# Kernel optimization log

Hardware: AMD Instinct MI355X
Metric: run time of the kernel (lower is better)

Reference implementation:

```python
import jax, jax.numpy as jnp
import numpy as np

N_NODES = 50000
N_EDGES = 1000000


def _edge_conv(x, src, dst, W, b, n_nodes):
    """PyG EdgeConv: msg = nn(cat([x_i, x_j - x_i])), aggr=max over incoming edges."""
    xi = x[dst]                      # [E, C] target features
    xj = x[src]                      # [E, C] source features
    m = jnp.concatenate([xi, xj - xi], axis=-1)          # [E, 2C]
    m = jax.nn.relu(m @ W + b)                           # [E, C_out]
    out = jax.ops.segment_max(m, dst, num_segments=n_nodes)  # [N, C_out]
    # empty segments produce -inf; PyG fills with 0
    return jnp.where(jnp.isfinite(out), out, 0.0)


def setup_inputs() -> dict:
    key = jax.random.key(0)
    ks = jax.random.split(key, 12)
    x = jax.random.normal(ks[0], (N_NODES, 3), dtype=jnp.float32)
    edge_index = jax.random.randint(ks[1], (2, N_EDGES), 0, N_NODES, dtype=jnp.int64)

    def lin(k, fan_in, fan_out):
        s = 1.0 / np.sqrt(fan_in)
        kw, kb = jax.random.split(k)
        W = jax.random.uniform(kw, (fan_in, fan_out), jnp.float32, -s, s)
        b = jax.random.uniform(kb, (fan_out,), jnp.float32, -s, s)
        return W, b

    W1, b1 = lin(ks[2], 6, 64)       # conv1 MLP([3*2, 64])
    W2, b2 = lin(ks[3], 128, 128)    # conv2 MLP([64*2, 128])
    W3, b3 = lin(ks[4], 256, 512)    # conv3 MLP([128*2, 512])
    W4, b4 = lin(ks[5], 512, 256)    # lin1 MLP([512, 256])
    W5, b5 = lin(ks[6], 256, 3)      # lin1 final Linear(256, 3)
    return {"x": x, "edge_index": edge_index,
            "W1": W1, "b1": b1, "W2": W2, "b2": b2, "W3": W3, "b3": b3,
            "W4": W4, "b4": b4, "W5": W5, "b5": b5}


def reference(x, edge_index, W1, b1, W2, b2, W3, b3, W4, b4, W5, b5):
    src = edge_index[0]  # x_j
    dst = edge_index[1]  # x_i (aggregation target)
    n = x.shape[0]
    x1 = _edge_conv(x, src, dst, W1, b1, n)    # [N, 64]
    x2 = _edge_conv(x1, src, dst, W2, b2, n)   # [N, 128]
    x3 = _edge_conv(x2, src, dst, W3, b3, n)   # [N, 512]
    x4 = jax.nn.relu(x3 @ W4 + b4) @ W5 + b5   # [N, 3]
    return x + x4
```

## Files before the change

kernel.cpp:

```cpp
#include <hip/hip_runtime.h>

static constexpr int NN = 50000;
static constexpr int NE = 1000000;

typedef short bf16x8 __attribute__((ext_vector_type(8)));
typedef float f32x4 __attribute__((ext_vector_type(4)));

__device__ inline float bf2f_raw(unsigned short u) {
    return __uint_as_float(((unsigned int)u) << 16);
}
__device__ inline unsigned short f2bf(float f) {
    unsigned int u = __float_as_uint(f);
    u += 0x7fffu + ((u >> 16) & 1u);
    return (unsigned short)(u >> 16);
}
__device__ inline void fmax2(float& a0, float& a1, unsigned int v) {
    a0 = fmaxf(a0, bf2f_raw((unsigned short)(v & 0xffffu)));
    a1 = fmaxf(a1, bf2f_raw((unsigned short)(v >> 16)));
}
__device__ inline unsigned int pack2(float f0, float f1) {
    return (unsigned int)f2bf(f0) | ((unsigned int)f2bf(f1) << 16);
}
__device__ inline unsigned int addrelu2(unsigned int a, float t0, float t1) {
    float f0 = fmaxf(bf2f_raw((unsigned short)(a & 0xffffu)) + t0, 0.f);
    float f1 = fmaxf(bf2f_raw((unsigned short)(a >> 16)) + t1, 0.f);
    return pack2(f0, f1);
}


__global__ void setup_kernel(const float* __restrict__ x, const float* __restrict__ W1,
                             const float* __restrict__ b1, const float* __restrict__ b5,
                             const float* __restrict__ W2, const float* __restrict__ W3,
                             const float* __restrict__ W4,
                             unsigned short* __restrict__ as1, float* __restrict__ out,
                             int* __restrict__ deg, int* __restrict__ cursor,
                             unsigned short* __restrict__ Bt2,
                             unsigned short* __restrict__ Bt3,
                             unsigned short* __restrict__ W4t) {
    int t = blockIdx.x * blockDim.x + threadIdx.x;
    if (t < NN * 128) {
        int i = t >> 7, c = t & 127;
        float x0 = x[i * 3 + 0], x1 = x[i * 3 + 1], x2 = x[i * 3 + 2];
        float v;
        if (c < 64) {
            v = x0 * (W1[c] - W1[192 + c]) + x1 * (W1[64 + c] - W1[256 + c]) +
                x2 * (W1[128 + c] - W1[320 + c]) + b1[c];
        } else {
            int cs = c - 64;
            v = x0 * W1[192 + cs] + x1 * W1[256 + cs] + x2 * W1[320 + cs];
        }
        as1[t] = f2bf(v);
        return;
    }
    t -= NN * 128;
    if (t < NN * 3) { out[t] = x[t] + b5[t % 3]; return; }
    t -= NN * 3;
    if (t < NN) { deg[t] = 0; return; }
    t -= NN;
    if (t < NN) { cursor[t] = 0; return; }
    t -= NN;
    if (t < 8192) {
        int k = t / 128, c = t % 128;
        float wt = W2[k * 128 + c];
        float wb = W2[(64 + k) * 128 + c];
        Bt2[c * 64 + k] = f2bf(wt - wb);
        Bt2[(128 + c) * 64 + k] = f2bf(wb);
        return;
    }
    t -= 8192;
    if (t < 65536) {
        int k = t / 512, c = t % 512;
        float wt = W3[k * 512 + c];
        float wb = W3[(128 + k) * 512 + c];
        Bt3[c * 128 + k] = f2bf(wt - wb);
        Bt3[(512 + c) * 128 + k] = f2bf(wb);
        return;
    }
    t -= 65536;
    if (t < 131072) {
        int k = t / 256, n = t % 256;
        W4t[n * 512 + k] = f2bf(W4[k * 256 + n]);
    }
}


__global__ void hist_kernel(const int* __restrict__ dst, int* __restrict__ deg) {
    int e = blockIdx.x * blockDim.x + threadIdx.x;
    if (e < NE) atomicAdd(&deg[dst[e]], 1);
}

__global__ __launch_bounds__(1024) void scan_kernel(const int* __restrict__ deg,
                                                    int* __restrict__ rowstart) {
    __shared__ int wave_sums[16];
    constexpr int CH = (NN + 1023) / 1024;
    int tid = threadIdx.x;
    int lane = tid & 63;
    int wave = tid >> 6;
    int base = tid * CH;
    int vals[CH];
    int sum = 0;
    #pragma unroll
    for (int i = 0; i < CH; ++i) {
        int idx = base + i;
        vals[i] = (idx < NN) ? deg[idx] : 0;
        sum += vals[i];
    }
    int x = sum;
    #pragma unroll
    for (int off = 1; off < 64; off <<= 1) {
        int y = __shfl_up(x, off);
        if (lane >= off) x += y;
    }
    if (lane == 63) wave_sums[wave] = x;
    __syncthreads();
    if (wave == 0 && lane < 16) {
        int s = wave_sums[lane];
        #pragma unroll
        for (int off = 1; off < 16; off <<= 1) {
            int y = __shfl_up(s, off);
            if (lane >= off) s += y;
        }
        wave_sums[lane] = s;
    }
    __syncthreads();
    int run = (wave ? wave_sums[wave - 1] : 0) + x - sum;
    #pragma unroll
    for (int i = 0; i < CH; ++i) {
        int idx = base + i;
        if (idx < NN) rowstart[idx] = run;
        run += vals[i];
    }
    if (tid == 1023) rowstart[NN] = run;
}

__global__ void scatter_kernel(const int* __restrict__ src, const int* __restrict__ dst,
                               const int* __restrict__ rowstart, int* __restrict__ cursor,
                               int* __restrict__ csr) {
    int e = blockIdx.x * blockDim.x + threadIdx.x;
    if (e < NE) {
        int d = dst[e];
        int pos = atomicAdd(&cursor[d], 1);
        csr[rowstart[d] + pos] = src[e];
    }
}


__global__ __launch_bounds__(256) void edge_fused_conv1_kernel(
    const unsigned short* __restrict__ as, const int* __restrict__ rowstart,
    const int* __restrict__ csr, unsigned short* __restrict__ x1) {
    int wid = (blockIdx.x * 256 + threadIdx.x) >> 6;
    int lane = threadIdx.x & 63;
    if (wid >= NN) return;
    int e0 = __builtin_amdgcn_readfirstlane(rowstart[wid]);
    int e1 = __builtin_amdgcn_readfirstlane(rowstart[wid + 1]);
    int h = lane >> 5, c0 = (lane & 31) * 2;
    float t0 = -INFINITY, t1 = -INFINITY;
    const unsigned short* sb = as + 64 + c0;
    int nedge = e1 - e0;
    for (int base = 0; base < nedge; base += 64) {
        int rem = nedge - base;
        int myj = csr[(lane < rem) ? (e0 + base + lane) : e0];
        int cnt = rem < 64 ? rem : 64;
        int cp = (cnt + 7) & ~7;
        for (int q = 0; q < cp; q += 8) {
            int j0 = __shfl(myj, q + 0 + h);
            int j1 = __shfl(myj, q + 2 + h);
            int j2 = __shfl(myj, q + 4 + h);
            int j3 = __shfl(myj, q + 6 + h);
            unsigned int v0 = *(const unsigned int*)(sb + (size_t)j0 * 128);
            unsigned int v1 = *(const unsigned int*)(sb + (size_t)j1 * 128);
            unsigned int v2 = *(const unsigned int*)(sb + (size_t)j2 * 128);
            unsigned int v3 = *(const unsigned int*)(sb + (size_t)j3 * 128);
            fmax2(t0, t1, v0);
            fmax2(t0, t1, v1);
            fmax2(t0, t1, v2);
            fmax2(t0, t1, v3);
        }
    }
    t0 = fmaxf(t0, __shfl_xor(t0, 32));
    t1 = fmaxf(t1, __shfl_xor(t1, 32));
    if (h == 0) {
        unsigned int av = *(const unsigned int*)(as + (size_t)wid * 128 + c0);
        *(unsigned int*)(x1 + (size_t)wid * 64 + c0) = addrelu2(av, t0, t1);
    }
}


__global__ __launch_bounds__(256) void edge_fused128_kernel(
    const unsigned short* __restrict__ as, const int* __restrict__ rowstart,
    const int* __restrict__ csr, unsigned short* __restrict__ xout) {
    int wid = (blockIdx.x * 256 + threadIdx.x) >> 6;
    int lane = threadIdx.x & 63;
    if (wid >= NN) return;
    int e0 = __builtin_amdgcn_readfirstlane(rowstart[wid]);
    int e1 = __builtin_amdgcn_readfirstlane(rowstart[wid + 1]);
    float t0 = -INFINITY, t1 = -INFINITY;
    const unsigned short* sb = as + 128 + (size_t)lane * 2;
    int nedge = e1 - e0;
    for (int base = 0; base < nedge; base += 64) {
        int rem = nedge - base;
        int myj = csr[(lane < rem) ? (e0 + base + lane) : e0];
        int cnt = rem < 64 ? rem : 64;
        int cp = (cnt + 7) & ~7;
        for (int q = 0; q < cp; q += 8) {
            int j0 = __shfl(myj, q + 0), j1 = __shfl(myj, q + 1);
            int j2 = __shfl(myj, q + 2), j3 = __shfl(myj, q + 3);
            int j4 = __shfl(myj, q + 4), j5 = __shfl(myj, q + 5);
            int j6 = __shfl(myj, q + 6), j7 = __shfl(myj, q + 7);
            unsigned int v0 = *(const unsigned int*)(sb + (size_t)j0 * 256);
            unsigned int v1 = *(const unsigned int*)(sb + (size_t)j1 * 256);
            unsigned int v2 = *(const unsigned int*)(sb + (size_t)j2 * 256);
            unsigned int v3 = *(const unsigned int*)(sb + (size_t)j3 * 256);
            unsigned int v4 = *(const unsigned int*)(sb + (size_t)j4 * 256);
            unsigned int v5 = *(const unsigned int*)(sb + (size_t)j5 * 256);
            unsigned int v6 = *(const unsigned int*)(sb + (size_t)j6 * 256);
            unsigned int v7 = *(const unsigned int*)(sb + (size_t)j7 * 256);
            fmax2(t0, t1, v0); fmax2(t0, t1, v1);
            fmax2(t0, t1, v2); fmax2(t0, t1, v3);
            fmax2(t0, t1, v4); fmax2(t0, t1, v5);
            fmax2(t0, t1, v6); fmax2(t0, t1, v7);
        }
    }
    unsigned int av = *(const unsigned int*)(as + (size_t)wid * 256 + lane * 2);
    *(unsigned int*)(xout + (size_t)wid * 128 + lane * 2) = addrelu2(av, t0, t1);
}


__global__ __launch_bounds__(256) void ef512_w5_kernel(
    const unsigned short* __restrict__ as, const int* __restrict__ rowstart,
    const int* __restrict__ csr, const unsigned short* __restrict__ W4t,
    const float* __restrict__ b4, const float* __restrict__ W5,
    float* __restrict__ out) {
    __shared__ __align__(16) unsigned short X[16][520];
    int wave = threadIdx.x >> 6, lane = threadIdx.x & 63;
    int tilebase = blockIdx.x * 16;

    const unsigned short* sb = as + 512 + (size_t)lane * 8;
    for (int i = 0; i < 4; ++i) {
        int node = tilebase + wave * 4 + i;
        int e0 = __builtin_amdgcn_readfirstlane(rowstart[node]);
        int e1 = __builtin_amdgcn_readfirstlane(rowstart[node + 1]);
        float acc[8];
        #pragma unroll
        for (int v = 0; v < 8; ++v) acc[v] = -INFINITY;
        int nedge = e1 - e0;
        for (int base = 0; base < nedge; base += 64) {
            int rem = nedge - base;
            int myj = csr[(lane < rem) ? (e0 + base + lane) : e0];
            int cnt = rem < 64 ? rem : 64;
            int cp = (cnt + 3) & ~3;
            for (int q = 0; q < cp; q += 4) {
                int j0 = __shfl(myj, q + 0), j1 = __shfl(myj, q + 1);
                int j2 = __shfl(myj, q + 2), j3 = __shfl(myj, q + 3);
                uint4 v0 = *(const uint4*)(sb + (size_t)j0 * 1024);
                uint4 v1 = *(const uint4*)(sb + (size_t)j1 * 1024);
                uint4 v2 = *(const uint4*)(sb + (size_t)j2 * 1024);
                uint4 v3 = *(const uint4*)(sb + (size_t)j3 * 1024);
                fmax2(acc[0], acc[1], v0.x); fmax2(acc[2], acc[3], v0.y);
                fmax2(acc[4], acc[5], v0.z); fmax2(acc[6], acc[7], v0.w);
                fmax2(acc[0], acc[1], v1.x); fmax2(acc[2], acc[3], v1.y);
                fmax2(acc[4], acc[5], v1.z); fmax2(acc[6], acc[7], v1.w);
                fmax2(acc[0], acc[1], v2.x); fmax2(acc[2], acc[3], v2.y);
                fmax2(acc[4], acc[5], v2.z); fmax2(acc[6], acc[7], v2.w);
                fmax2(acc[0], acc[1], v3.x); fmax2(acc[2], acc[3], v3.y);
                fmax2(acc[4], acc[5], v3.z); fmax2(acc[6], acc[7], v3.w);
            }
        }
        uint4 av = *(const uint4*)(as + (size_t)node * 1024 + lane * 8);
        uint4 o;
        o.x = addrelu2(av.x, acc[0], acc[1]);
        o.y = addrelu2(av.y, acc[2], acc[3]);
        o.z = addrelu2(av.z, acc[4], acc[5]);
        o.w = addrelu2(av.w, acc[6], acc[7]);
        *(uint4*)&X[wave * 4 + i][lane * 8] = o;
    }
    __syncthreads();

    int quad = lane >> 4, l16 = lane & 15;
    int colbase = wave * 64;
    f32x4 acc4[4] = {};
    for (int kc = 0; kc < 16; ++kc) {
        bf16x8 afr = *(const bf16x8*)&X[l16][kc * 32 + quad * 8];
        #pragma unroll
        for (int nt = 0; nt < 4; ++nt) {
            int col = colbase + nt * 16 + l16;
            bf16x8 bfr = *(const bf16x8*)&W4t[(size_t)col * 512 + kc * 32 + quad * 8];
            acc4[nt] = __builtin_amdgcn_mfma_f32_16x16x32_bf16(afr, bfr, acc4[nt], 0, 0, 0);
        }
    }
    float b4v[4], w5r[4][3];
    #pragma unroll
    for (int nt = 0; nt < 4; ++nt) {
        int col = colbase + nt * 16 + l16;
        b4v[nt] = b4[col];
        w5r[nt][0] = W5[col * 3 + 0];
        w5r[nt][1] = W5[col * 3 + 1];
        w5r[nt][2] = W5[col * 3 + 2];
    }
    #pragma unroll
    for (int r = 0; r < 4; ++r) {
        int row = tilebase + quad * 4 + r;
        float p0 = 0.f, p1 = 0.f, p2 = 0.f;
        #pragma unroll
        for (int nt = 0; nt < 4; ++nt) {
            float h = fmaxf(acc4[nt][r] + b4v[nt], 0.f);
            p0 += h * w5r[nt][0];
            p1 += h * w5r[nt][1];
            p2 += h * w5r[nt][2];
        }
        #pragma unroll
        for (int m = 8; m; m >>= 1) {
            p0 += __shfl_xor(p0, m);
            p1 += __shfl_xor(p1, m);
            p2 += __shfl_xor(p2, m);
        }
        if (l16 == 0) {
            atomicAdd(&out[row * 3 + 0], p0);
            atomicAdd(&out[row * 3 + 1], p1);
            atomicAdd(&out[row * 3 + 2], p2);
        }
    }
}


template<int K, int NT>
__global__ __launch_bounds__(256) void mfma_gemm_nloop_kernel(
    const unsigned short* __restrict__ A, const unsigned short* __restrict__ Bt,
    const float* __restrict__ bias, int bias_n,
    unsigned short* __restrict__ C, int M) {
    constexpr int KC = K / 32;
    constexpr int N = NT * 128;
    __shared__ __align__(16) unsigned short Asl[KC][128 * 40];
    __shared__ __align__(16) unsigned short Bsl[128 * 40];
    int tid = threadIdx.x;
    int mbase = blockIdx.x * 128;
    int wave = tid >> 6, lane = tid & 63;
    int wm = (wave >> 1) * 64, wn = (wave & 1) * 64;
    int quad = lane >> 4, l16 = lane & 15;

    #pragma unroll
    for (int c = tid; c < KC * 512; c += 256) {
        int kc = c >> 9, rem = c & 511;
        int r = rem >> 2, kk = (rem & 3) * 8;
        uint4 va = make_uint4(0u, 0u, 0u, 0u);
        int gr = mbase + r;
        if (gr < M) va = *(const uint4*)&A[(size_t)gr * K + kc * 32 + kk];
        *(uint4*)&Asl[kc][r * 40 + kk] = va;
    }

    for (int nt = 0; nt < NT; ++nt) {
        int nbase = nt * 128;
        f32x4 acc[4][4] = {};
        for (int kc = 0; kc < KC; ++kc) {
            __syncthreads();
            #pragma unroll
            for (int h = 0; h < 2; ++h) {
                int c = tid + h * 256;
                int r = c >> 2, kk = (c & 3) * 8;
                uint4 vb = *(const uint4*)&Bt[(size_t)(nbase + r) * K + kc * 32 + kk];
                *(uint4*)&Bsl[r * 40 + kk] = vb;
            }
            __syncthreads();
            bf16x8 af[4], bfr[4];
            #pragma unroll
            for (int tt = 0; tt < 4; ++tt) {
                af[tt]  = *(const bf16x8*)&Asl[kc][(wm + tt * 16 + l16) * 40 + quad * 8];
                bfr[tt] = *(const bf16x8*)&Bsl[(wn + tt * 16 + l16) * 40 + quad * 8];
            }
            #pragma unroll
            for (int mt = 0; mt < 4; ++mt)
                #pragma unroll
                for (int ntt = 0; ntt < 4; ++ntt)
                    acc[mt][ntt] = __builtin_amdgcn_mfma_f32_16x16x32_bf16(
                        af[mt], bfr[ntt], acc[mt][ntt], 0, 0, 0);
        }
        #pragma unroll
        for (int mt = 0; mt < 4; ++mt) {
            #pragma unroll
            for (int r = 0; r < 4; ++r) {
                int row = mbase + wm + mt * 16 + quad * 4 + r;
                if (row >= M) continue;
                #pragma unroll
                for (int ntt = 0; ntt < 4; ++ntt) {
                    int col = nbase + wn + ntt * 16 + l16;
                    float v = acc[mt][ntt][r];
                    if (col < bias_n) v += bias[col];
                    C[(size_t)row * N + col] = f2bf(v);
                }
            }
        }
    }
}

__global__ void fallback_copy_kernel(const float* __restrict__ x, float* __restrict__ out) {
    int t = blockIdx.x * blockDim.x + threadIdx.x;
    if (t < NN * 3) out[t] = x[t];
}


extern "C" void kernel_launch(void* const* d_in, const int* in_sizes, int n_in,
                              void* d_out, int out_size, void* d_ws, size_t ws_size,
                              hipStream_t stream) {
    const float* x  = (const float*)d_in[0];
    const int*   ei = (const int*)d_in[1];
    const float* W1 = (const float*)d_in[2];
    const float* b1 = (const float*)d_in[3];
    const float* W2 = (const float*)d_in[4];
    const float* b2 = (const float*)d_in[5];
    const float* W3 = (const float*)d_in[6];
    const float* b3 = (const float*)d_in[7];
    const float* W4 = (const float*)d_in[8];
    const float* b4 = (const float*)d_in[9];
    const float* W5 = (const float*)d_in[10];
    const float* b5 = (const float*)d_in[11];
    float* out = (float*)d_out;

    char* p = (char*)d_ws;
    auto alloc = [&](size_t bytes) -> void* {
        void* r = (void*)p;
        p += (bytes + 255) & ~(size_t)255;
        return r;
    };
    int* deg      = (int*)alloc((size_t)NN * 4);
    int* rowstart = (int*)alloc((size_t)(NN + 1) * 4);
    int* cursor   = (int*)alloc((size_t)NN * 4);
    int* csr      = (int*)alloc((size_t)NE * 4);
    unsigned short* Bt2 = (unsigned short*)alloc(256 * 64 * 2);
    unsigned short* Bt3 = (unsigned short*)alloc(1024 * 128 * 2);
    unsigned short* W4t = (unsigned short*)alloc(256 * 512 * 2);
    unsigned short* x1 = (unsigned short*)alloc((size_t)NN * 64 * 2);
    unsigned short* x2 = (unsigned short*)alloc((size_t)NN * 128 * 2);
    unsigned short* as_slab = (unsigned short*)alloc((size_t)NN * 1024 * 2);
    size_t need = (size_t)(p - (char*)d_ws);
    if (ws_size < need) {
        fallback_copy_kernel<<<(NN * 3 + 255) / 256, 256, 0, stream>>>(x, out);
        return;
    }

    const int* src = ei;
    const int* dst = ei + NE;

    constexpr int SETUP_T = NN * 128 + NN * 3 + NN + NN + 8192 + 65536 + 131072;
    setup_kernel<<<(SETUP_T + 255) / 256, 256, 0, stream>>>(
        x, W1, b1, b5, W2, W3, W4, as_slab, out, deg, cursor, Bt2, Bt3, W4t);

    hist_kernel<<<(NE + 255) / 256, 256, 0, stream>>>(dst, deg);
    scan_kernel<<<1, 1024, 0, stream>>>(deg, rowstart);
    scatter_kernel<<<(NE + 255) / 256, 256, 0, stream>>>(src, dst, rowstart, cursor, csr);

    edge_fused_conv1_kernel<<<12500, 256, 0, stream>>>(as_slab, rowstart, csr, x1);

    mfma_gemm_nloop_kernel<64, 2><<<391, 256, 0, stream>>>(
        x1, Bt2, b2, 128, as_slab, NN);
    edge_fused128_kernel<<<12500, 256, 0, stream>>>(as_slab, rowstart, csr, x2);

    mfma_gemm_nloop_kernel<128, 8><<<391, 256, 0, stream>>>(
        x2, Bt3, b3, 512, as_slab, NN);

    ef512_w5_kernel<<<NN / 16, 256, 0, stream>>>(
        as_slab, rowstart, csr, W4t, b4, W5, out);
}
```

Before: 602.0 us.

## Store gathered halves as order-preserving sortable bf16 keys and use packed integer max

The gathered (source-side) half of each projection is now stored in a sign-flipped sortable bf16 encoding, so the max-aggregation can run as packed unsigned 16-bit integer max instead of unpack-to-float plus fmaxf per element. The producer GEMM epilogue and setup kernel emit this encoding, and the consumer decodes it only once per node before the add/ReLU. The gather loops are also restructured to software-pipeline the next batch of loads ahead of the max reductions. The aim is fewer ALU ops per gathered element and better load latency hiding. Empty segments now start from zero keys, which decode to NaN or a negative value instead of -inf, so the handling of zero-degree nodes may differ.

```diff
diff --git a/kernel.cpp b/kernel.cpp
--- a/kernel.cpp
+++ b/kernel.cpp
@@ -5,6 +5,7 @@
 
 typedef short bf16x8 __attribute__((ext_vector_type(8)));
 typedef float f32x4 __attribute__((ext_vector_type(4)));
+typedef unsigned short u16x2 __attribute__((ext_vector_type(2)));
 
 __device__ inline float bf2f_raw(unsigned short u) {
     return __uint_as_float(((unsigned int)u) << 16);
@@ -14,14 +15,26 @@
     u += 0x7fffu + ((u >> 16) & 1u);
     return (unsigned short)(u >> 16);
 }
-__device__ inline void fmax2(float& a0, float& a1, unsigned int v) {
-    a0 = fmaxf(a0, bf2f_raw((unsigned short)(v & 0xffffu)));
-    a1 = fmaxf(a1, bf2f_raw((unsigned short)(v >> 16)));
+__device__ inline unsigned short f2bfs(float f) {
+    unsigned short b = f2bf(f);
+    return (b & 0x8000u) ? (unsigned short)(~b) : (unsigned short)(b | 0x8000u);
+}
+__device__ inline float unsrt2f(unsigned short v) {
+    unsigned short b = (v & 0x8000u) ? (unsigned short)(v ^ 0x8000u)
+                                     : (unsigned short)(~v);
+    return bf2f_raw(b);
+}
+__device__ inline unsigned int pkmax(unsigned int a, unsigned int b) {
+    u16x2 r = __builtin_elementwise_max(__builtin_bit_cast(u16x2, a),
+                                        __builtin_bit_cast(u16x2, b));
+    return __builtin_bit_cast(unsigned int, r);
 }
 __device__ inline unsigned int pack2(float f0, float f1) {
     return (unsigned int)f2bf(f0) | ((unsigned int)f2bf(f1) << 16);
 }
-__device__ inline unsigned int addrelu2(unsigned int a, float t0, float t1) {
+__device__ inline unsigned int addrelu2t(unsigned int a, unsigned int t) {
+    float t0 = unsrt2f((unsigned short)(t & 0xffffu));
+    float t1 = unsrt2f((unsigned short)(t >> 16));
     float f0 = fmaxf(bf2f_raw((unsigned short)(a & 0xffffu)) + t0, 0.f);
     float f1 = fmaxf(bf2f_raw((unsigned short)(a >> 16)) + t1, 0.f);
     return pack2(f0, f1);
@@ -41,15 +54,15 @@
     if (t < NN * 128) {
         int i = t >> 7, c = t & 127;
         float x0 = x[i * 3 + 0], x1 = x[i * 3 + 1], x2 = x[i * 3 + 2];
-        float v;
         if (c < 64) {
-            v = x0 * (W1[c] - W1[192 + c]) + x1 * (W1[64 + c] - W1[256 + c]) +
-                x2 * (W1[128 + c] - W1[320 + c]) + b1[c];
+            float v = x0 * (W1[c] - W1[192 + c]) + x1 * (W1[64 + c] - W1[256 + c]) +
+                      x2 * (W1[128 + c] - W1[320 + c]) + b1[c];
+            as1[t] = f2bf(v);
         } else {
             int cs = c - 64;
-            v = x0 * W1[192 + cs] + x1 * W1[256 + cs] + x2 * W1[320 + cs];
-        }
-        as1[t] = f2bf(v);
+            float v = x0 * W1[192 + cs] + x1 * W1[256 + cs] + x2 * W1[320 + cs];
+            as1[t] = f2bfs(v);
+        }
         return;
     }
     t -= NN * 128;
@@ -154,7 +167,7 @@
     int e0 = __builtin_amdgcn_readfirstlane(rowstart[wid]);
     int e1 = __builtin_amdgcn_readfirstlane(rowstart[wid + 1]);
     int h = lane >> 5, c0 = (lane & 31) * 2;
-    float t0 = -INFINITY, t1 = -INFINITY;
+    unsigned int t = 0u;
     const unsigned short* sb = as + 64 + c0;
     int nedge = e1 - e0;
     for (int base = 0; base < nedge; base += 64) {
@@ -162,26 +175,31 @@
         int myj = csr[(lane < rem) ? (e0 + base + lane) : e0];
         int cnt = rem < 64 ? rem : 64;
         int cp = (cnt + 7) & ~7;
-        for (int q = 0; q < cp; q += 8) {
-            int j0 = __shfl(myj, q + 0 + h);
-            int j1 = __shfl(myj, q + 2 + h);
-            int j2 = __shfl(myj, q + 4 + h);
-            int j3 = __shfl(myj, q + 6 + h);
-            unsigned int v0 = *(const unsigned int*)(sb + (size_t)j0 * 128);
-            unsigned int v1 = *(const unsigned int*)(sb + (size_t)j1 * 128);
-            unsigned int v2 = *(const unsigned int*)(sb + (size_t)j2 * 128);
-            unsigned int v3 = *(const unsigned int*)(sb + (size_t)j3 * 128);
-            fmax2(t0, t1, v0);
-            fmax2(t0, t1, v1);
-            fmax2(t0, t1, v2);
-            fmax2(t0, t1, v3);
-        }
-    }
-    t0 = fmaxf(t0, __shfl_xor(t0, 32));
-    t1 = fmaxf(t1, __shfl_xor(t1, 32));
+        unsigned int v[4];
+        #pragma unroll
+        for (int k = 0; k < 4; ++k) {
+            int j = __shfl(myj, 2 * k + h);
+            v[k] = *(const unsigned int*)(sb + (size_t)j * 128);
+        }
+        for (int q = 8; q < cp; q += 8) {
+            unsigned int w[4];
+            #pragma unroll
+            for (int k = 0; k < 4; ++k) {
+                int j = __shfl(myj, q + 2 * k + h);
+                w[k] = *(const unsigned int*)(sb + (size_t)j * 128);
+            }
+            #pragma unroll
+            for (int k = 0; k < 4; ++k) t = pkmax(t, v[k]);
+            #pragma unroll
+            for (int k = 0; k < 4; ++k) v[k] = w[k];
+        }
+        #pragma unroll
+        for (int k = 0; k < 4; ++k) t = pkmax(t, v[k]);
+    }
+    t = pkmax(t, __shfl_xor(t, 32));
     if (h == 0) {
         unsigned int av = *(const unsigned int*)(as + (size_t)wid * 128 + c0);
-        *(unsigned int*)(x1 + (size_t)wid * 64 + c0) = addrelu2(av, t0, t1);
+        *(unsigned int*)(x1 + (size_t)wid * 64 + c0) = addrelu2t(av, t);
     }
 }
 
@@ -194,7 +212,7 @@
     if (wid >= NN) return;
     int e0 = __builtin_amdgcn_readfirstlane(rowstart[wid]);
     int e1 = __builtin_amdgcn_readfirstlane(rowstart[wid + 1]);
-    float t0 = -INFINITY, t1 = -INFINITY;
+    unsigned int t = 0u;
     const unsigned short* sb = as + 128 + (size_t)lane * 2;
     int nedge = e1 - e0;
     for (int base = 0; base < nedge; base += 64) {
@@ -202,27 +220,29 @@
         int myj = csr[(lane < rem) ? (e0 + base + lane) : e0];
         int cnt = rem < 64 ? rem : 64;
         int cp = (cnt + 7) & ~7;
-        for (int q = 0; q < cp; q += 8) {
-            int j0 = __shfl(myj, q + 0), j1 = __shfl(myj, q + 1);
-            int j2 = __shfl(myj, q + 2), j3 = __shfl(myj, q + 3);
-            int j4 = __shfl(myj, q + 4), j5 = __shfl(myj, q + 5);
-            int j6 = __shfl(myj, q + 6), j7 = __shfl(myj, q + 7);
-            unsigned int v0 = *(const unsigned int*)(sb + (size_t)j0 * 256);
-            unsigned int v1 = *(const unsigned int*)(sb + (size_t)j1 * 256);
-            unsigned int v2 = *(const unsigned int*)(sb + (size_t)j2 * 256);
-            unsigned int v3 = *(const unsigned int*)(sb + (size_t)j3 * 256);
-            unsigned int v4 = *(const unsigned int*)(sb + (size_t)j4 * 256);
-            unsigned int v5 = *(const unsigned int*)(sb + (size_t)j5 * 256);
-            unsigned int v6 = *(const unsigned int*)(sb + (size_t)j6 * 256);
-            unsigned int v7 = *(const unsigned int*)(sb + (size_t)j7 * 256);
-            fmax2(t0, t1, v0); fmax2(t0, t1, v1);
-            fmax2(t0, t1, v2); fmax2(t0, t1, v3);
-            fmax2(t0, t1, v4); fmax2(t0, t1, v5);
-            fmax2(t0, t1, v6); fmax2(t0, t1, v7);
-        }
+        unsigned int v[8];
+        #pragma unroll
+        for (int k = 0; k < 8; ++k) {
+            int j = __shfl(myj, k);
+            v[k] = *(const unsigned int*)(sb + (size_t)j * 256);
+        }
+        for (int q = 8; q < cp; q += 8) {
+            unsigned int w[8];
+            #pragma unroll
+            for (int k = 0; k < 8; ++k) {
+                int j = __shfl(myj, q + k);
+                w[k] = *(const unsigned int*)(sb + (size_t)j * 256);
+            }
+            #pragma unroll
+            for (int k = 0; k < 8; ++k) t = pkmax(t, v[k]);
+            #pragma unroll
+            for (int k = 0; k < 8; ++k) v[k] = w[k];
+        }
+        #pragma unroll
+        for (int k = 0; k < 8; ++k) t = pkmax(t, v[k]);
     }
     unsigned int av = *(const unsigned int*)(as + (size_t)wid * 256 + lane * 2);
-    *(unsigned int*)(xout + (size_t)wid * 128 + lane * 2) = addrelu2(av, t0, t1);
+    *(unsigned int*)(xout + (size_t)wid * 128 + lane * 2) = addrelu2t(av, t);
 }
 
 
@@ -240,38 +260,51 @@
         int node = tilebase + wave * 4 + i;
         int e0 = __builtin_amdgcn_readfirstlane(rowstart[node]);
         int e1 = __builtin_amdgcn_readfirstlane(rowstart[node + 1]);
-        float acc[8];
-        #pragma unroll
-        for (int v = 0; v < 8; ++v) acc[v] = -INFINITY;
+        unsigned int m0 = 0u, m1 = 0u, m2 = 0u, m3 = 0u;
         int nedge = e1 - e0;
         for (int base = 0; base < nedge; base += 64) {
             int rem = nedge - base;
             int myj = csr[(lane < rem) ? (e0 + base + lane) : e0];
             int cnt = rem < 64 ? rem : 64;
             int cp = (cnt + 3) & ~3;
-            for (int q = 0; q < cp; q += 4) {
-                int j0 = __shfl(myj, q + 0), j1 = __shfl(myj, q + 1);
-                int j2 = __shfl(myj, q + 2), j3 = __shfl(myj, q + 3);
-                uint4 v0 = *(const uint4*)(sb + (size_t)j0 * 1024);
-                uint4 v1 = *(const uint4*)(sb + (size_t)j1 * 1024);
-                uint4 v2 = *(const uint4*)(sb + (size_t)j2 * 1024);
-                uint4 v3 = *(const uint4*)(sb + (size_t)j3 * 1024);
-                fmax2(acc[0], acc[1], v0.x); fmax2(acc[2], acc[3], v0.y);
-                fmax2(acc[4], acc[5], v0.z); fmax2(acc[6], acc[7], v0.w);
-                fmax2(acc[0], acc[1], v1.x); fmax2(acc[2], acc[3], v1.y);
-                fmax2(acc[4], acc[5], v1.z); fmax2(acc[6], acc[7], v1.w);
-                fmax2(acc[0], acc[1], v2.x); fmax2(acc[2], acc[3], v2.y);
-                fmax2(acc[4], acc[5], v2.z); fmax2(acc[6], acc[7], v2.w);
-                fmax2(acc[0], acc[1], v3.x); fmax2(acc[2], acc[3], v3.y);
-                fmax2(acc[4], acc[5], v3.z); fmax2(acc[6], acc[7], v3.w);
-            }
+            int j0 = __shfl(myj, 0), j1 = __shfl(myj, 1);
+            int j2 = __shfl(myj, 2), j3 = __shfl(myj, 3);
+            uint4 v0 = *(const uint4*)(sb + (size_t)j0 * 1024);
+            uint4 v1 = *(const uint4*)(sb + (size_t)j1 * 1024);
+            uint4 v2 = *(const uint4*)(sb + (size_t)j2 * 1024);
+            uint4 v3 = *(const uint4*)(sb + (size_t)j3 * 1024);
+            for (int q = 4; q < cp; q += 4) {
+                int k0 = __shfl(myj, q + 0), k1 = __shfl(myj, q + 1);
+                int k2 = __shfl(myj, q + 2), k3 = __shfl(myj, q + 3);
+                uint4 w0 = *(const uint4*)(sb + (size_t)k0 * 1024);
+                uint4 w1 = *(const uint4*)(sb + (size_t)k1 * 1024);
+                uint4 w2 = *(const uint4*)(sb + (size_t)k2 * 1024);
+                uint4 w3 = *(const uint4*)(sb + (size_t)k3 * 1024);
+                m0 = pkmax(m0, v0.x); m1 = pkmax(m1, v0.y);
+                m2 = pkmax(m2, v0.z); m3 = pkmax(m3, v0.w);
+                m0 = pkmax(m0, v1.x); m1 = pkmax(m1, v1.y);
+                m2 = pkmax(m2, v1.z); m3 = pkmax(m3, v1.w);
+                m0 = pkmax(m0, v2.x); m1 = pkmax(m1, v2.y);
+                m2 = pkmax(m2, v2.z); m3 = pkmax(m3, v2.w);
+                m0 = pkmax(m0, v3.x); m1 = pkmax(m1, v3.y);
+                m2 = pkmax(m2, v3.z); m3 = pkmax(m3, v3.w);
+                v0 = w0; v1 = w1; v2 = w2; v3 = w3;
+            }
+            m0 = pkmax(m0, v0.x); m1 = pkmax(m1, v0.y);
+            m2 = pkmax(m2, v0.z); m3 = pkmax(m3, v0.w);
+            m0 = pkmax(m0, v1.x); m1 = pkmax(m1, v1.y);
+            m2 = pkmax(m2, v1.z); m3 = pkmax(m3, v1.w);
+            m0 = pkmax(m0, v2.x); m1 = pkmax(m1, v2.y);
+            m2 = pkmax(m2, v2.z); m3 = pkmax(m3, v2.w);
+            m0 = pkmax(m0, v3.x); m1 = pkmax(m1, v3.y);
+            m2 = pkmax(m2, v3.z); m3 = pkmax(m3, v3.w);
         }
         uint4 av = *(const uint4*)(as + (size_t)node * 1024 + lane * 8);
         uint4 o;
-        o.x = addrelu2(av.x, acc[0], acc[1]);
-        o.y = addrelu2(av.y, acc[2], acc[3]);
-        o.z = addrelu2(av.z, acc[4], acc[5]);
-        o.w = addrelu2(av.w, acc[6], acc[7]);
+        o.x = addrelu2t(av.x, m0);
+        o.y = addrelu2t(av.y, m1);
+        o.z = addrelu2t(av.z, m2);
+        o.w = addrelu2t(av.w, m3);
         *(uint4*)&X[wave * 4 + i][lane * 8] = o;
     }
     __syncthreads();
@@ -384,8 +417,10 @@
                 for (int ntt = 0; ntt < 4; ++ntt) {
                     int col = nbase + wn + ntt * 16 + l16;
                     float v = acc[mt][ntt][r];
-                    if (col < bias_n) v += bias[col];
-                    C[(size_t)row * N + col] = f2bf(v);
+                    unsigned short o;
+                    if (col < bias_n) o = f2bf(v + bias[col]);
+                    else o = f2bfs(v);
+                    C[(size_t)row * N + col] = o;
                 }
             }
         }
```

New measurement: 597.9 us. Within noise of the previous version (-0.7%).
